# Performance work log

Hardware: AMD Instinct MI355X
Metric: run time of the kernel (lower is better)

The kernel has to match this reference:

```python
import jax, jax.numpy as jnp
import numpy as np

B, S, D_MODEL = 2, 2048, 1024
HID, D_FF, H, WIN = 256, 512, 4, 9
LN_EPS = 1e-5


def setup_inputs() -> dict:
    key = jax.random.key(0)
    ks = jax.random.split(key, 12)
    w = lambda k, shape: jax.random.normal(k, shape, jnp.float32) * 0.02
    return dict(
        q=jax.random.normal(ks[0], (B, S, D_MODEL), jnp.float32),
        k=jax.random.normal(ks[1], (B, S, D_MODEL), jnp.float32),
        v=jax.random.normal(ks[2], (B, S, D_MODEL), jnp.float32),
        Wq=w(ks[3], (D_MODEL, HID)), bq=jnp.zeros((HID,), jnp.float32),
        Wk=w(ks[4], (D_MODEL, HID)), bk=jnp.zeros((HID,), jnp.float32),
        Wv=w(ks[5], (D_MODEL, HID)), bv=jnp.zeros((HID,), jnp.float32),
        Wo=w(ks[6], (HID, D_MODEL)), bo=jnp.zeros((D_MODEL,), jnp.float32),
        alpha=jnp.zeros((1,), jnp.float32),
        adj_w=jnp.full((1,), 0.6, jnp.float32),
        adj_b=jnp.full((1,), 0.2, jnp.float32),
        W1=w(ks[7], (D_MODEL, D_FF)), b1=jnp.zeros((D_FF,), jnp.float32),
        W2=w(ks[8], (D_FF, D_MODEL)), b2=jnp.zeros((D_MODEL,), jnp.float32),
        g1=jnp.ones((D_MODEL,), jnp.float32), be1=jnp.zeros((D_MODEL,), jnp.float32),
        g2=jnp.ones((D_MODEL,), jnp.float32), be2=jnp.zeros((D_MODEL,), jnp.float32),
    )


def _layernorm(x, g, b):
    mu = jnp.mean(x, axis=-1, keepdims=True)
    var = jnp.mean((x - mu) ** 2, axis=-1, keepdims=True)
    return (x - mu) * jax.lax.rsqrt(var + LN_EPS) * g + b


def _signed_sqrt(x):
    # sqrt(relu(x)) - sqrt(relu(-x)) with torch-style zero grad on masked branch
    p = jnp.where(x > 0, jnp.sqrt(jnp.where(x > 0, x, 1.0)), 0.0)
    n = jnp.where(x < 0, jnp.sqrt(jnp.where(x < 0, -x, 1.0)), 0.0)
    return p - n


def _local_mask(seq_len, win):
    j = jnp.arange(seq_len)[:, None]              # [S,1]
    kk = jnp.arange(win)[None, :]                 # [1,W]
    idx = jnp.clip(j - win // 2 + kk, 0, seq_len - 1)
    m = jnp.zeros((seq_len, seq_len), jnp.float32)
    return m.at[jnp.broadcast_to(j, (seq_len, win)), idx].set(1.0)


def _forward(q, k, v, Wq, bq, Wk, bk, Wv, bv, Wo, bo, alpha, adj_w, adj_b,
             W1, b1, W2, b2, g1, be1, g2, be2):
    bs, seq, _ = q.shape
    dh = HID // H
    scale = 1.0 / np.sqrt(HID)

    Q = (q @ Wq + bq).reshape(bs, seq, H, dh).transpose(0, 2, 1, 3)  # [B,H,S,dh]
    K = (k @ Wk + bk).reshape(bs, seq, H, dh).transpose(0, 2, 1, 3)
    V = (v @ Wv + bv).reshape(bs, seq, H, dh).transpose(0, 2, 1, 3)

    # distance adjacency bias: exp(-|w*d^2 - b|), d = |i-j|
    i = jnp.arange(seq, dtype=jnp.float32)
    dist = jnp.abs(i[:, None] - i[None, :])
    adj = jnp.exp(-jnp.abs(adj_w[0] * dist ** 2 - adj_b[0]))  # [S,S]

    scores = jnp.einsum('bhqd,bhkd->bhqk', Q, K) * scale + adj  # [B,H,S,S]

    mask = _local_mask(seq, WIN)                                 # [S,S]
    l_scores = jnp.where(mask == 0, -1e9, scores)

    g_map = jax.nn.softmax(scores, axis=-1)
    l_map = jax.nn.softmax(l_scores, axis=-1)

    glb = jnp.einsum('bhqk,bhkd->bqhd', g_map, V).reshape(bs, seq, HID)
    lcl = jnp.einsum('bhqk,bhkd->bqhd', l_map, V).reshape(bs, seq, HID)

    a = jax.nn.sigmoid(alpha[0])
    tmp = a * glb + (1.0 - a) * lcl

    # norm_flag: signed sqrt then F.normalize (L2 along dim=1, eps=1e-12)
    tmp = _signed_sqrt(tmp)
    nrm = jnp.maximum(jnp.sqrt(jnp.sum(tmp ** 2, axis=1, keepdims=True)), 1e-12)
    tmp = tmp / nrm

    attn_out = tmp @ Wo + bo

    x = q + attn_out
    x = _layernorm(x, g1, be1)
    # FFN (dropout inactive in eval)
    x = x + (jax.nn.relu(x @ W1 + b1) @ W2 + b2)
    x = _layernorm(x, g2, be2)
    return x


def reference(q, k, v, Wq, bq, Wk, bk, Wv, bv, Wo, bo, alpha, adj_w, adj_b,
              W1, b1, W2, b2, g1, be1, g2, be2):
    return _forward(q, k, v, Wq, bq, Wk, bk, Wv, bv, Wo, bo, alpha, adj_w,
                    adj_b, W1, b1, W2, b2, g1, be1, g2, be2)
```

## Files before the change

kernel.cpp:

```cpp
#include <hip/hip_runtime.h>

#define B_SZ   2
#define S_LEN  2048
#define DMODEL 1024
#define HID    256
#define NH     4
#define DH     64
#define DFF    512
#define LN_EPS 1e-5f
#define ATT_SCALE 0.0625f

typedef __attribute__((ext_vector_type(8))) short bf16x8;
typedef __attribute__((ext_vector_type(4))) float f32x4;

static __device__ __forceinline__ unsigned short f2bf(float x) {
    union { float f; unsigned u; } v; v.f = x;
    unsigned r = v.u + 0x7FFFu + ((v.u >> 16) & 1u);
    return (unsigned short)(r >> 16);
}
static __device__ __forceinline__ unsigned packbf(float a, float b) {
    return (unsigned)f2bf(a) | ((unsigned)f2bf(b) << 16);
}
static __device__ __forceinline__ float bf2f(unsigned short h) {
    union { unsigned u; float f; } v; v.u = ((unsigned)h) << 16; return v.f;
}
static __device__ __forceinline__ int swz(int byte) {
    return byte ^ ((byte >> 3) & 0x70);
}

#if defined(__has_builtin)
#if __has_builtin(__builtin_amdgcn_global_load_lds)
#define HAVE_GLD 1
#endif
#endif

static __device__ __forceinline__ void gld16(const void* g, void* l) {
#ifdef HAVE_GLD
    __builtin_amdgcn_global_load_lds(
        (const __attribute__((address_space(1))) void*)g,
        (__attribute__((address_space(3))) void*)l, 16, 0, 0);
#else
    *(uint4*)((char*)l + (threadIdx.x & 63) * 16) = *(const uint4*)g;
#endif
}

__device__ __forceinline__ void stage_tile(const unsigned short* __restrict__ G,
                                           int row0, int k0, int K, char* lds, int t)
{
    #pragma unroll
    for (int i = 0; i < 2; ++i) {
        int ci = (t >> 6) * 2 + i;
        int o  = (ci * 64 + (t & 63)) * 16;
        int L  = o ^ ((o >> 3) & 0x70);
        const char* ga = (const char*)G +
            ((size_t)(row0 + (L >> 7)) * K + k0) * 2 + (L & 127);
        gld16(ga, lds + ci * 1024);
    }
}

__device__ __forceinline__ void compute_strip(const char* As, const char* Bs,
                                              f32x4 acc[4], int w, int lr, int lg)
{
    #pragma unroll
    for (int ks = 0; ks < 2; ++ks) {
        int koff = ks * 64 + lg * 16;
        bf16x8 bfv = *(const bf16x8*)(Bs + (((w * 16 + lr) * 128 + koff) ^ ((lr & 7) << 4)));
        #pragma unroll
        for (int m = 0; m < 4; ++m) {
            int r = m * 16 + lr;
            bf16x8 af = *(const bf16x8*)(As + ((r * 128 + koff) ^ ((lr & 7) << 4)));
            acc[m] = __builtin_amdgcn_mfma_f32_16x16x32_bf16(af, bfv, acc[m], 0, 0, 0);
        }
    }
}

__device__ __forceinline__ void gemm64_core(
    const unsigned short* __restrict__ A, const unsigned short* __restrict__ W,
    const float* __restrict__ bias, const float* __restrict__ residf,
    const unsigned short* __restrict__ residb,
    float* __restrict__ Cf, unsigned short* __restrict__ Cb,
    int N, int K, int relu, int row0, int col0)
{
    __shared__ char ldsb[32768];
    char* As0 = ldsb;          char* Bs0 = ldsb + 8192;
    char* As1 = ldsb + 16384;  char* Bs1 = ldsb + 24576;

    const int t = threadIdx.x;
    const int w = t >> 6, l = t & 63;
    const int lr = l & 15, lg = l >> 4;

    f32x4 acc[4] = {};

    stage_tile(A, row0, 0, K, As0, t);
    stage_tile(W, col0, 0, K, Bs0, t);
    __syncthreads();

    const int NK = K >> 6;
    int buf = 0;
    for (int ks = 0; ks < NK; ++ks) {
        if (ks + 1 < NK) {
            stage_tile(A, row0, (ks + 1) * 64, K, buf ? As0 : As1, t);
            stage_tile(W, col0, (ks + 1) * 64, K, buf ? Bs0 : Bs1, t);
        }
        compute_strip(buf ? As1 : As0, buf ? Bs1 : Bs0, acc, w, lr, lg);
        __syncthreads();
        buf ^= 1;
    }

    float* T = (float*)ldsb;
    #pragma unroll
    for (int m = 0; m < 4; ++m)
        #pragma unroll
        for (int r = 0; r < 4; ++r)
            T[(m * 16 + lg * 4 + r) * 65 + w * 16 + lr] =
                acc[m][r] + bias[col0 + w * 16 + lr];
    __syncthreads();

    #pragma unroll
    for (int i = 0; i < 4; ++i) {
        int idx = t + i * 256;
        int row = idx >> 4, c4 = idx & 15;
        float v0 = T[row * 65 + c4 * 4 + 0];
        float v1 = T[row * 65 + c4 * 4 + 1];
        float v2 = T[row * 65 + c4 * 4 + 2];
        float v3 = T[row * 65 + c4 * 4 + 3];
        size_t goff = (size_t)(row0 + row) * N + col0 + c4 * 4;
        if (residf) {
            float4 rv = *(const float4*)(residf + goff);
            v0 += rv.x; v1 += rv.y; v2 += rv.z; v3 += rv.w;
        }
        if (residb) {
            uint2 rb = *(const uint2*)(residb + goff);
            v0 += bf2f((unsigned short)(rb.x & 0xFFFF));
            v1 += bf2f((unsigned short)(rb.x >> 16));
            v2 += bf2f((unsigned short)(rb.y & 0xFFFF));
            v3 += bf2f((unsigned short)(rb.y >> 16));
        }
        if (relu) {
            v0 = fmaxf(v0, 0.f); v1 = fmaxf(v1, 0.f);
            v2 = fmaxf(v2, 0.f); v3 = fmaxf(v3, 0.f);
        }
        if (Cb) *(uint2*)(Cb + goff) = make_uint2(packbf(v0, v1), packbf(v2, v3));
        else    *(float4*)(Cf + goff) = make_float4(v0, v1, v2, v3);
    }
}

__global__ __launch_bounds__(256) void gemm_b16(
    const unsigned short* __restrict__ A, const unsigned short* __restrict__ W,
    const float* __restrict__ bias, const float* __restrict__ residf,
    const unsigned short* __restrict__ residb,
    float* __restrict__ Cf, unsigned short* __restrict__ Cb,
    int N, int K, int relu)
{
    gemm64_core(A, W, bias, residf, residb, Cf, Cb, N, K, relu,
                blockIdx.x * 64, blockIdx.y * 64);
}

__global__ __launch_bounds__(256) void gemm_qkv3(
    const unsigned short* __restrict__ qkvb, const unsigned short* __restrict__ Wt,
    const float* __restrict__ bq, const float* __restrict__ bk,
    const float* __restrict__ bv, unsigned short* __restrict__ outb)
{
    const int z = blockIdx.z;
    const unsigned short* A = qkvb + (size_t)z * 4096 * 1024;
    const unsigned short* W = Wt + (size_t)z * 262144;
    const float* bias = (z == 0) ? bq : ((z == 1) ? bk : bv);
    unsigned short* Cb = outb + (size_t)z * 4096 * 256;
    gemm64_core(A, W, bias, nullptr, nullptr, nullptr, Cb, 256, 1024, 0,
                blockIdx.x * 64, blockIdx.y * 64);
}

__global__ __launch_bounds__(256) void prep_w(
    const float* __restrict__ Wq, const float* __restrict__ Wk,
    const float* __restrict__ Wv, const float* __restrict__ Wo,
    const float* __restrict__ W1, const float* __restrict__ W2,
    unsigned short* __restrict__ Wt)
{
    __shared__ float tile[64][65];
    const int bid = blockIdx.x;
    const float* src; int K, N; size_t off; int local;
    if (bid < 64)       { src = Wq; K = 1024; N = 256;  off = 0;        local = bid; }
    else if (bid < 128) { src = Wk; K = 1024; N = 256;  off = 262144;  local = bid - 64; }
    else if (bid < 192) { src = Wv; K = 1024; N = 256;  off = 524288;  local = bid - 128; }
    else if (bid < 256) { src = Wo; K = 256;  N = 1024; off = 786432;  local = bid - 192; }
    else if (bid < 384) { src = W1; K = 1024; N = 512;  off = 1048576; local = bid - 256; }
    else                { src = W2; K = 512;  N = 1024; off = 1572864; local = bid - 384; }
    const int nkt = K >> 6;
    const int k0 = (local % nkt) * 64, n0 = (local / nkt) * 64;
    const int t = threadIdx.x;
    #pragma unroll
    for (int i = 0; i < 16; ++i) {
        int id = t + i * 256;
        int r = id >> 6, c = id & 63;
        tile[r][c] = src[(size_t)(k0 + r) * N + n0 + c];
    }
    __syncthreads();
    unsigned* Wt32 = (unsigned*)(Wt + off);
    #pragma unroll
    for (int i = 0; i < 8; ++i) {
        int id = t + i * 256;
        int n = id >> 5, ku = id & 31;
        Wt32[((size_t)(n0 + n) * K + k0) / 2 + ku] =
            packbf(tile[2 * ku][n], tile[2 * ku + 1][n]);
    }
}

__global__ __launch_bounds__(256) void prep_qkv(
    const float* __restrict__ q, const float* __restrict__ k,
    const float* __restrict__ v, unsigned short* __restrict__ qkvb)
{
    const float* src = blockIdx.z == 0 ? q : (blockIdx.z == 1 ? k : v);
    uint2* dst = (uint2*)(qkvb + (size_t)blockIdx.z * 4096 * 1024);
    int idx = blockIdx.x * 256 + threadIdx.x;
    float4 x = ((const float4*)src)[idx];
    dst[idx] = make_uint2(packbf(x.x, x.y), packbf(x.z, x.w));
}

__global__ __launch_bounds__(256) void prep_v(const unsigned short* __restrict__ Vb,
                                              unsigned short* __restrict__ Vt)
{
    __shared__ unsigned Vl[64][34];
    const int k0 = blockIdx.x * 64;
    const int bh = blockIdx.y;
    const int b = bh >> 2, h = bh & 3;
    const int t = threadIdx.x;
    const unsigned* Vg = (const unsigned*)Vb + (size_t)(b * S_LEN) * 128 + h * 32;
    #pragma unroll
    for (int i = 0; i < 8; ++i) {
        int id = t + i * 256;
        int key = id >> 5, cu = id & 31;
        Vl[key][cu] = Vg[(size_t)(k0 + key) * 128 + cu];
    }
    __syncthreads();
    const unsigned short* Vl16 = (const unsigned short*)Vl;
    unsigned* Vo = (unsigned*)Vt + (size_t)bh * 65536;
    #pragma unroll
    for (int i = 0; i < 8; ++i) {
        int id = t + i * 256;
        int d = id >> 5, ku = id & 31;
        unsigned lo = Vl16[(2 * ku) * 68 + d];
        unsigned hi = Vl16[(2 * ku + 1) * 68 + d];
        Vo[(size_t)d * 1024 + (k0 >> 1) + ku] = lo | (hi << 16);
    }
}

__global__ __launch_bounds__(256) void attn_global_split(
    const unsigned short* __restrict__ Qb, const unsigned short* __restrict__ Kb,
    const unsigned short* __restrict__ Vt, const float* __restrict__ adj_w,
    const float* __restrict__ adj_b, float* __restrict__ Opart,
    float* __restrict__ mlpart)
{
    __shared__ unsigned Kl[2048];
    __shared__ unsigned Vl[2048];
    __shared__ unsigned Pl[4][512];

    const int q0 = blockIdx.x * 64;
    const int bh = blockIdx.y;
    const int ck = blockIdx.z;
    const int b = bh >> 2, h = bh & 3;
    const int t = threadIdx.x;
    const int w = t >> 6, l = t & 63;
    const int lr = l & 15, lg = l >> 4;
    const float aw = adj_w[0], ab = adj_b[0];

    const int qrow = q0 + w * 16 + lr;
    const unsigned* qb32 = (const unsigned*)Qb + (size_t)(b * S_LEN + qrow) * 128 + h * 32;
    bf16x8 qf[2];
    #pragma unroll
    for (int hh = 0; hh < 2; ++hh) {
        union { unsigned u[4]; bf16x8 v; } tmpu;
        #pragma unroll
        for (int jj = 0; jj < 4; ++jj) tmpu.u[jj] = qb32[hh * 16 + lg * 4 + jj];
        qf[hh] = tmpu.v;
    }

    const unsigned* Kg = (const unsigned*)Kb + (size_t)(b * S_LEN) * 128 + h * 32;
    const unsigned* Vg = (const unsigned*)Vt + (size_t)bh * 65536;
    const int kbase = ck * 512;

    float mrow = -1e30f, lrow = 0.f;
    f32x4 o[4] = {};
    uint4 rk[2], rv[2];

    #pragma unroll
    for (int i = 0; i < 2; ++i) {
        int id4 = t + i * 256;
        int r4 = id4 >> 3, c4 = id4 & 7;
        rk[i] = *(const uint4*)(Kg + (size_t)(kbase + r4) * 128 + c4 * 4);
        rv[i] = *(const uint4*)(Vg + (size_t)r4 * 1024 + (kbase >> 1) + c4 * 4);
    }
    #pragma unroll
    for (int i = 0; i < 2; ++i) {
        int id4 = t + i * 256;
        int r4 = id4 >> 3, c4 = id4 & 7;
        *(uint4*)((char*)Kl + swz(r4 * 128 + c4 * 16)) = rk[i];
        *(uint4*)((char*)Vl + swz(r4 * 128 + c4 * 16)) = rv[i];
    }

    for (int tt = 0; tt < 8; ++tt) {
        const int k0 = kbase + tt * 64;
        __syncthreads();
        if (tt < 7) {
            const int kn = k0 + 64;
            #pragma unroll
            for (int i = 0; i < 2; ++i) {
                int id4 = t + i * 256;
                int r4 = id4 >> 3, c4 = id4 & 7;
                rk[i] = *(const uint4*)(Kg + (size_t)(kn + r4) * 128 + c4 * 4);
                rv[i] = *(const uint4*)(Vg + (size_t)r4 * 1024 + (kn >> 1) + c4 * 4);
            }
        }

        float sv[4][4];
        #pragma unroll
        for (int f = 0; f < 4; ++f) {
            int krow = f * 16 + lr;
            bf16x8 kf0 = *(const bf16x8*)((const char*)Kl + swz(krow * 128 + lg * 16));
            bf16x8 kf1 = *(const bf16x8*)((const char*)Kl + swz(krow * 128 + lg * 16 + 64));
            f32x4 stf = {0.f, 0.f, 0.f, 0.f};
            stf = __builtin_amdgcn_mfma_f32_16x16x32_bf16(kf0, qf[0], stf, 0, 0, 0);
            stf = __builtin_amdgcn_mfma_f32_16x16x32_bf16(kf1, qf[1], stf, 0, 0, 0);
            int klo = k0 + f * 16;
            bool near = (q0 + w * 16 + 15 >= klo - 6) && (q0 + w * 16 <= klo + 21);
            #pragma unroll
            for (int r = 0; r < 4; ++r) {
                float x = stf[r] * ATT_SCALE;
                if (near) {
                    int key = klo + lg * 4 + r;
                    float dd = (float)(qrow - key);
                    x += __expf(-fabsf(aw * dd * dd - ab));
                }
                sv[f][r] = x;
            }
        }

        float tmax = -1e30f;
        #pragma unroll
        for (int f = 0; f < 4; ++f)
            #pragma unroll
            for (int r = 0; r < 4; ++r) tmax = fmaxf(tmax, sv[f][r]);
        tmax = fmaxf(tmax, __shfl_xor(tmax, 16, 64));
        tmax = fmaxf(tmax, __shfl_xor(tmax, 32, 64));
        float mnew = fmaxf(mrow, tmax);
        float fac  = __expf(mrow - mnew);
        float ts = 0.f;
        #pragma unroll
        for (int f = 0; f < 4; ++f)
            #pragma unroll
            for (int r = 0; r < 4; ++r) {
                float p = __expf(sv[f][r] - mnew);
                sv[f][r] = p; ts += p;
            }
        ts += __shfl_xor(ts, 16, 64);
        ts += __shfl_xor(ts, 32, 64);
        lrow = lrow * fac + ts;
        mrow = mnew;
        #pragma unroll
        for (int rf = 0; rf < 4; ++rf) o[rf] *= fac;

        #pragma unroll
        for (int f = 0; f < 4; ++f) {
            uint2 pw;
            pw.x = packbf(sv[f][0], sv[f][1]);
            pw.y = packbf(sv[f][2], sv[f][3]);
            *(uint2*)((char*)Pl[w] + swz(lr * 128 + f * 32 + lg * 8)) = pw;
        }

        #pragma unroll
        for (int hh = 0; hh < 2; ++hh) {
            bf16x8 pf = *(const bf16x8*)((const char*)Pl[w] + swz(lr * 128 + lg * 16 + 64 * hh));
            #pragma unroll
            for (int rf = 0; rf < 4; ++rf) {
                int vrow = rf * 16 + lr;
                bf16x8 vf = *(const bf16x8*)((const char*)Vl + swz(vrow * 128 + lg * 16 + 64 * hh));
                o[rf] = __builtin_amdgcn_mfma_f32_16x16x32_bf16(vf, pf, o[rf], 0, 0, 0);
            }
        }

        __syncthreads();
        if (tt < 7) {
            #pragma unroll
            for (int i = 0; i < 2; ++i) {
                int id4 = t + i * 256;
                int r4 = id4 >> 3, c4 = id4 & 7;
                *(uint4*)((char*)Kl + swz(r4 * 128 + c4 * 16)) = rk[i];
                *(uint4*)((char*)Vl + swz(r4 * 128 + c4 * 16)) = rv[i];
            }
        }
    }

    const size_t idx = (size_t)(ck * 8 + bh) * 2048 + qrow;
    float* op = Opart + idx * 64;
    #pragma unroll
    for (int rf = 0; rf < 4; ++rf)
        *(float4*)(op + rf * 16 + lg * 4) = make_float4(o[rf][0], o[rf][1], o[rf][2], o[rf][3]);
    if (lg == 0) {
        mlpart[idx * 2]     = mrow;
        mlpart[idx * 2 + 1] = lrow;
    }
}

__global__ __launch_bounds__(256) void attn_combine(
    const float* __restrict__ Opart, const float* __restrict__ mlpart,
    const unsigned short* __restrict__ lcl_b, const float* __restrict__ alpha,
    unsigned short* __restrict__ tmpb)
{
    const int row = blockIdx.x;
    const int b = row >> 11;
    const int w = threadIdx.x >> 6;
    const int lane = threadIdx.x & 63;
    const size_t base = (size_t)(b * NH + w) * 2048 + (row & 2047);

    float mv[4], lv[4];
    float M = -1e30f;
    #pragma unroll
    for (int ck = 0; ck < 4; ++ck) {
        mv[ck] = mlpart[(ck * 16384 + base) * 2];
        lv[ck] = mlpart[(ck * 16384 + base) * 2 + 1];
        M = fmaxf(M, mv[ck]);
    }
    float O = 0.f, L = 0.f;
    #pragma unroll
    for (int ck = 0; ck < 4; ++ck) {
        float e = __expf(mv[ck] - M);
        O += e * Opart[(ck * 16384 + base) * 64 + lane];
        L += e * lv[ck];
    }
    float g = O / L;
    float lval = bf2f(lcl_b[(size_t)row * HID + w * 64 + lane]);
    float a = 1.f / (1.f + expf(-alpha[0]));
    float x = a * g + (1.f - a) * lval;
    float r = x > 0.f ? sqrtf(x) : (x < 0.f ? -sqrtf(-x) : 0.f);
    tmpb[(size_t)row * HID + w * 64 + lane] = f2bf(r);
}

__global__ __launch_bounds__(256) void attn_local(
    const unsigned short* __restrict__ Qb, const unsigned short* __restrict__ Kb,
    const unsigned short* __restrict__ Vb, const float* __restrict__ adj_w,
    const float* __restrict__ adj_b, unsigned short* __restrict__ lcl_b)
{
    const int wave = threadIdx.x >> 6;
    const int lane = threadIdx.x & 63;
    const int gr = blockIdx.x * 4 + wave;
    const int b = gr >> 13;
    const int rem = gr & 8191;
    const int h = rem >> 11;
    const int i = rem & 2047;
    const float w = adj_w[0], bb = adj_b[0];

    const float qd = bf2f(Qb[(size_t)(b * S_LEN + i) * HID + h * 64 + lane]);

    float sc[9]; int cls[9];
    float mx = -1e30f; int prev = -1;
    #pragma unroll
    for (int kk = 0; kk < 9; ++kk) {
        int c = i - 4 + kk;
        c = c < 0 ? 0 : (c > S_LEN - 1 ? S_LEN - 1 : c);
        bool valid = (c != prev);
        prev = c;
        float kd = bf2f(Kb[(size_t)(b * S_LEN + c) * HID + h * 64 + lane]);
        float part = qd * kd;
        #pragma unroll
        for (int off = 32; off; off >>= 1) part += __shfl_xor(part, off, 64);
        float dd = fabsf((float)(i - c));
        float vv = part * ATT_SCALE + expf(-fabsf(w * dd * dd - bb));
        sc[kk]  = valid ? vv : -1e30f;
        cls[kk] = c;
        mx = fmaxf(mx, sc[kk]);
    }
    float sum = 0.f;
    #pragma unroll
    for (int kk = 0; kk < 9; ++kk) { sc[kk] = expf(sc[kk] - mx); sum += sc[kk]; }
    const float inv = 1.f / sum;
    float o = 0.f;
    #pragma unroll
    for (int kk = 0; kk < 9; ++kk)
        o += sc[kk] * bf2f(Vb[(size_t)(b * S_LEN + cls[kk]) * HID + h * 64 + lane]);

    lcl_b[((size_t)(b * S_LEN + i)) * HID + h * 64 + lane] = f2bf(o * inv);
}

__global__ __launch_bounds__(256) void colnorm_part(
    const unsigned short* __restrict__ tmpb, float* __restrict__ part)
{
    __shared__ unsigned short Tl[16][256];
    const int b = blockIdx.x >> 7, ch = blockIdx.x & 127;
    const int t = threadIdx.x;
    const uint4* src = (const uint4*)(tmpb + ((size_t)b * S_LEN + ch * 16) * HID);
    #pragma unroll
    for (int i = 0; i < 2; ++i) {
        int idx = t + i * 256;
        ((uint4*)Tl)[idx] = src[idx];
    }
    __syncthreads();
    float ss = 0.f;
    #pragma unroll
    for (int r = 0; r < 16; ++r) {
        float v2 = bf2f(Tl[r][t]);
        ss += v2 * v2;
    }
    part[blockIdx.x * 256 + t] = ss;
}

__global__ __launch_bounds__(64) void colnorm_fin(
    const float* __restrict__ part, float* __restrict__ inv_nrm)
{
    const int bc = blockIdx.x;
    const int b = bc >> 8, c = bc & 255;
    const int j = threadIdx.x;
    float s = part[(b * 128 + j) * 256 + c] + part[(b * 128 + j + 64) * 256 + c];
    #pragma unroll
    for (int off = 32; off; off >>= 1) s += __shfl_xor(s, off, 64);
    if (j == 0) inv_nrm[bc] = 1.f / fmaxf(sqrtf(s), 1e-12f);
}

__global__ __launch_bounds__(256) void scale_inv(
    unsigned short* __restrict__ tmpb, const float* __restrict__ inv_nrm)
{
    int idx = blockIdx.x * 256 + threadIdx.x;
    int c = idx & 255, b = idx >> 19;
    tmpb[idx] = f2bf(bf2f(tmpb[idx]) * inv_nrm[b * 256 + c]);
}

__global__ __launch_bounds__(256) void layernorm_k(
    const float* __restrict__ x, const float* __restrict__ g,
    const float* __restrict__ be, float* __restrict__ outf,
    unsigned short* __restrict__ outb)
{
    const int row = blockIdx.x;
    const float4 xv = ((const float4*)(x + (size_t)row * DMODEL))[threadIdx.x];
    float s  = xv.x + xv.y + xv.z + xv.w;
    float ss = xv.x * xv.x + xv.y * xv.y + xv.z * xv.z + xv.w * xv.w;
    #pragma unroll
    for (int off = 32; off; off >>= 1) {
        s  += __shfl_xor(s,  off, 64);
        ss += __shfl_xor(ss, off, 64);
    }
    __shared__ float rs[4], rss[4];
    if ((threadIdx.x & 63) == 0) { rs[threadIdx.x >> 6] = s; rss[threadIdx.x >> 6] = ss; }
    __syncthreads();
    s  = rs[0] + rs[1] + rs[2] + rs[3];
    ss = rss[0] + rss[1] + rss[2] + rss[3];
    const float mu  = s * (1.f / DMODEL);
    const float var = ss * (1.f / DMODEL) - mu * mu;
    const float r   = rsqrtf(var + LN_EPS);
    const float4 gv = ((const float4*)g)[threadIdx.x];
    const float4 bv = ((const float4*)be)[threadIdx.x];
    float4 ov;
    ov.x = (xv.x - mu) * r * gv.x + bv.x;
    ov.y = (xv.y - mu) * r * gv.y + bv.y;
    ov.z = (xv.z - mu) * r * gv.z + bv.z;
    ov.w = (xv.w - mu) * r * gv.w + bv.w;
    if (outf) ((float4*)(outf + (size_t)row * DMODEL))[threadIdx.x] = ov;
    if (outb) {
        unsigned* ob = (unsigned*)(outb + (size_t)row * DMODEL);
        ob[threadIdx.x * 2]     = packbf(ov.x, ov.y);
        ob[threadIdx.x * 2 + 1] = packbf(ov.z, ov.w);
    }
}

extern "C" void kernel_launch(void* const* d_in, const int* in_sizes, int n_in,
                              void* d_out, int out_size, void* d_ws, size_t ws_size,
                              hipStream_t stream)
{
    const float* q     = (const float*)d_in[0];
    const float* k     = (const float*)d_in[1];
    const float* v     = (const float*)d_in[2];
    const float* Wq    = (const float*)d_in[3];
    const float* bq    = (const float*)d_in[4];
    const float* Wk    = (const float*)d_in[5];
    const float* bk    = (const float*)d_in[6];
    const float* Wv    = (const float*)d_in[7];
    const float* bv    = (const float*)d_in[8];
    const float* Wo    = (const float*)d_in[9];
    const float* bo    = (const float*)d_in[10];
    const float* alpha = (const float*)d_in[11];
    const float* adj_w = (const float*)d_in[12];
    const float* adj_b = (const float*)d_in[13];
    const float* W1    = (const float*)d_in[14];
    const float* b1    = (const float*)d_in[15];
    const float* W2    = (const float*)d_in[16];
    const float* b2    = (const float*)d_in[17];
    const float* g1    = (const float*)d_in[18];
    const float* be1   = (const float*)d_in[19];
    const float* g2    = (const float*)d_in[20];
    const float* be2   = (const float*)d_in[21];

    const int ROWS = B_SZ * S_LEN;

    char* WS = (char*)d_ws;
    float*          x1     = (float*)WS;
    float*          Opart  = (float*)WS;
    unsigned short* qkvb   = (unsigned short*)WS;
    float*          mlpart = (float*)(WS + (16u << 20));
    unsigned short* xlnb   = (unsigned short*)(WS + (16u << 20));
    unsigned short* lcl_b  = (unsigned short*)(WS + (26u << 20));
    unsigned short* Qb     = (unsigned short*)(WS + (28u << 20));
    unsigned short* Kb     = (unsigned short*)(WS + (30u << 20));
    unsigned short* Vb     = (unsigned short*)(WS + (32u << 20));
    unsigned short* Vt     = (unsigned short*)(WS + (34u << 20));
    unsigned short* tmpb   = (unsigned short*)(WS + (36u << 20));
    float*          invn   = (float*)(WS + (38u << 20));
    float*          part   = (float*)(WS + (38u << 20) + 4096);
    unsigned short* Wt     = (unsigned short*)(WS + (39u << 20));
    unsigned short* hbufb  = (unsigned short*)(WS + (28u << 20));

    prep_w<<<dim3(512), dim3(256), 0, stream>>>(Wq, Wk, Wv, Wo, W1, W2, Wt);
    prep_qkv<<<dim3(4096, 1, 3), dim3(256), 0, stream>>>(q, k, v, qkvb);
    gemm_qkv3<<<dim3(64, 4, 3), dim3(256), 0, stream>>>(qkvb, Wt, bq, bk, bv, Qb);
    prep_v<<<dim3(32, 8), dim3(256), 0, stream>>>(Vb, Vt);
    attn_global_split<<<dim3(32, 8, 4), dim3(256), 0, stream>>>(Qb, Kb, Vt, adj_w, adj_b,
                                                                Opart, mlpart);
    attn_local<<<dim3(4096), dim3(256), 0, stream>>>(Qb, Kb, Vb, adj_w, adj_b, lcl_b);
    attn_combine<<<dim3(4096), dim3(256), 0, stream>>>(Opart, mlpart, lcl_b, alpha, tmpb);
    colnorm_part<<<dim3(256), dim3(256), 0, stream>>>(tmpb, part);
    colnorm_fin<<<dim3(512), dim3(64), 0, stream>>>(part, invn);
    scale_inv<<<dim3(4096), dim3(256), 0, stream>>>(tmpb, invn);
    gemm_b16<<<dim3(64, 16), dim3(256), 0, stream>>>(tmpb, Wt + 786432, bo, q, nullptr,
                                                     x1, nullptr, DMODEL, HID, 0);
    layernorm_k<<<dim3(ROWS), dim3(256), 0, stream>>>(x1, g1, be1, nullptr, xlnb);
    gemm_b16<<<dim3(64, 8), dim3(256), 0, stream>>>(xlnb, Wt + 1048576, b1, nullptr, nullptr,
                                                    nullptr, hbufb, DFF, DMODEL, 1);
    gemm_b16<<<dim3(64, 16), dim3(256), 0, stream>>>(hbufb, Wt + 1572864, b2, nullptr, xlnb,
                                                     x1, nullptr, DMODEL, DFF, 0);
    layernorm_k<<<dim3(ROWS), dim3(256), 0, stream>>>(x1, g2, be2, (float*)d_out, nullptr);
}
```

Measured before the change: 268.3 us.

## Fuse local attention into combine, remap global-attention blocks, stage output via LDS

Merges the local windowed-attention kernel into the split-combine kernel, so the intermediate local result buffer is never written or re-read and one launch goes away. The global-attention grid is flattened to 1D with a swizzled block-to-tile mapping (bid&7 major) that groups blocks differently across XCDs/L2 for K/V reuse. Partial outputs are staged through shared memory and written as fully coalesced rows instead of scattered float4 stores. This costs extra syncthreads and a larger combine kernel with more registers.

```diff
diff --git a/kernel.cpp b/kernel.cpp
--- a/kernel.cpp
+++ b/kernel.cpp
@@ -250,13 +250,16 @@
     const float* __restrict__ adj_b, float* __restrict__ Opart,
     float* __restrict__ mlpart)
 {
-    __shared__ unsigned Kl[2048];
-    __shared__ unsigned Vl[2048];
-    __shared__ unsigned Pl[4][512];
-
-    const int q0 = blockIdx.x * 64;
-    const int bh = blockIdx.y;
-    const int ck = blockIdx.z;
+    __shared__ unsigned shmem[6144];
+    unsigned* Kl = shmem;
+    unsigned* Vl = shmem + 2048;
+    unsigned* Pl = shmem + 4096;
+
+    const int bid = blockIdx.x;
+    const int lid = (bid & 7) * 128 + (bid >> 3);
+    const int q0 = (lid & 31) * 64;
+    const int bh = (lid >> 5) & 7;
+    const int ck = lid >> 8;
     const int b = bh >> 2, h = bh & 3;
     const int t = threadIdx.x;
     const int w = t >> 6, l = t & 63;
@@ -363,12 +366,12 @@
             uint2 pw;
             pw.x = packbf(sv[f][0], sv[f][1]);
             pw.y = packbf(sv[f][2], sv[f][3]);
-            *(uint2*)((char*)Pl[w] + swz(lr * 128 + f * 32 + lg * 8)) = pw;
+            *(uint2*)((char*)(Pl + w * 512) + swz(lr * 128 + f * 32 + lg * 8)) = pw;
         }
 
         #pragma unroll
         for (int hh = 0; hh < 2; ++hh) {
-            bf16x8 pf = *(const bf16x8*)((const char*)Pl[w] + swz(lr * 128 + lg * 16 + 64 * hh));
+            bf16x8 pf = *(const bf16x8*)((const char*)(Pl + w * 512) + swz(lr * 128 + lg * 16 + 64 * hh));
             #pragma unroll
             for (int rf = 0; rf < 4; ++rf) {
                 int vrow = rf * 16 + lr;
@@ -376,7 +379,6 @@
                 o[rf] = __builtin_amdgcn_mfma_f32_16x16x32_bf16(vf, pf, o[rf], 0, 0, 0);
             }
         }
-
         __syncthreads();
         if (tt < 7) {
             #pragma unroll
@@ -390,71 +392,48 @@
     }
 
     const size_t idx = (size_t)(ck * 8 + bh) * 2048 + qrow;
-    float* op = Opart + idx * 64;
-    #pragma unroll
-    for (int rf = 0; rf < 4; ++rf)
-        *(float4*)(op + rf * 16 + lg * 4) = make_float4(o[rf][0], o[rf][1], o[rf][2], o[rf][3]);
     if (lg == 0) {
         mlpart[idx * 2]     = mrow;
         mlpart[idx * 2 + 1] = lrow;
     }
+
+    __syncthreads();
+    float* T = (float*)shmem;
+    #pragma unroll
+    for (int rf = 0; rf < 4; ++rf)
+        *(float4*)(T + (w * 16 + lr) * 68 + rf * 16 + lg * 4) =
+            make_float4(o[rf][0], o[rf][1], o[rf][2], o[rf][3]);
+    __syncthreads();
+    float* obase = Opart + ((size_t)(ck * 8 + bh) * 2048 + q0) * 64;
+    #pragma unroll
+    for (int i = 0; i < 4; ++i) {
+        int id = t + i * 256;
+        int row = id >> 4, c4 = id & 15;
+        *(float4*)(obase + row * 64 + c4 * 4) =
+            *(const float4*)(T + row * 68 + c4 * 4);
+    }
 }
 
 __global__ __launch_bounds__(256) void attn_combine(
     const float* __restrict__ Opart, const float* __restrict__ mlpart,
-    const unsigned short* __restrict__ lcl_b, const float* __restrict__ alpha,
+    const unsigned short* __restrict__ Qb, const unsigned short* __restrict__ Kb,
+    const unsigned short* __restrict__ Vb, const float* __restrict__ alpha,
+    const float* __restrict__ adj_w, const float* __restrict__ adj_b,
     unsigned short* __restrict__ tmpb)
 {
     const int row = blockIdx.x;
     const int b = row >> 11;
-    const int w = threadIdx.x >> 6;
+    const int s = row & 2047;
+    const int h = threadIdx.x >> 6;
     const int lane = threadIdx.x & 63;
-    const size_t base = (size_t)(b * NH + w) * 2048 + (row & 2047);
-
-    float mv[4], lv[4];
-    float M = -1e30f;
-    #pragma unroll
-    for (int ck = 0; ck < 4; ++ck) {
-        mv[ck] = mlpart[(ck * 16384 + base) * 2];
-        lv[ck] = mlpart[(ck * 16384 + base) * 2 + 1];
-        M = fmaxf(M, mv[ck]);
-    }
-    float O = 0.f, L = 0.f;
-    #pragma unroll
-    for (int ck = 0; ck < 4; ++ck) {
-        float e = __expf(mv[ck] - M);
-        O += e * Opart[(ck * 16384 + base) * 64 + lane];
-        L += e * lv[ck];
-    }
-    float g = O / L;
-    float lval = bf2f(lcl_b[(size_t)row * HID + w * 64 + lane]);
-    float a = 1.f / (1.f + expf(-alpha[0]));
-    float x = a * g + (1.f - a) * lval;
-    float r = x > 0.f ? sqrtf(x) : (x < 0.f ? -sqrtf(-x) : 0.f);
-    tmpb[(size_t)row * HID + w * 64 + lane] = f2bf(r);
-}
-
-__global__ __launch_bounds__(256) void attn_local(
-    const unsigned short* __restrict__ Qb, const unsigned short* __restrict__ Kb,
-    const unsigned short* __restrict__ Vb, const float* __restrict__ adj_w,
-    const float* __restrict__ adj_b, unsigned short* __restrict__ lcl_b)
-{
-    const int wave = threadIdx.x >> 6;
-    const int lane = threadIdx.x & 63;
-    const int gr = blockIdx.x * 4 + wave;
-    const int b = gr >> 13;
-    const int rem = gr & 8191;
-    const int h = rem >> 11;
-    const int i = rem & 2047;
     const float w = adj_w[0], bb = adj_b[0];
 
-    const float qd = bf2f(Qb[(size_t)(b * S_LEN + i) * HID + h * 64 + lane]);
-
+    const float qd = bf2f(Qb[(size_t)row * HID + h * 64 + lane]);
     float sc[9]; int cls[9];
     float mx = -1e30f; int prev = -1;
     #pragma unroll
     for (int kk = 0; kk < 9; ++kk) {
-        int c = i - 4 + kk;
+        int c = s - 4 + kk;
         c = c < 0 ? 0 : (c > S_LEN - 1 ? S_LEN - 1 : c);
         bool valid = (c != prev);
         prev = c;
@@ -462,7 +441,7 @@
         float part = qd * kd;
         #pragma unroll
         for (int off = 32; off; off >>= 1) part += __shfl_xor(part, off, 64);
-        float dd = fabsf((float)(i - c));
+        float dd = fabsf((float)(s - c));
         float vv = part * ATT_SCALE + expf(-fabsf(w * dd * dd - bb));
         sc[kk]  = valid ? vv : -1e30f;
         cls[kk] = c;
@@ -471,13 +450,33 @@
     float sum = 0.f;
     #pragma unroll
     for (int kk = 0; kk < 9; ++kk) { sc[kk] = expf(sc[kk] - mx); sum += sc[kk]; }
-    const float inv = 1.f / sum;
-    float o = 0.f;
+    float lval = 0.f;
     #pragma unroll
     for (int kk = 0; kk < 9; ++kk)
-        o += sc[kk] * bf2f(Vb[(size_t)(b * S_LEN + cls[kk]) * HID + h * 64 + lane]);
-
-    lcl_b[((size_t)(b * S_LEN + i)) * HID + h * 64 + lane] = f2bf(o * inv);
+        lval += sc[kk] * bf2f(Vb[(size_t)(b * S_LEN + cls[kk]) * HID + h * 64 + lane]);
+    lval /= sum;
+
+    const size_t base = (size_t)(b * NH + h) * 2048 + s;
+    float mv[4], lv[4];
+    float M = -1e30f;
+    #pragma unroll
+    for (int ck = 0; ck < 4; ++ck) {
+        mv[ck] = mlpart[(ck * 16384 + base) * 2];
+        lv[ck] = mlpart[(ck * 16384 + base) * 2 + 1];
+        M = fmaxf(M, mv[ck]);
+    }
+    float O = 0.f, L = 0.f;
+    #pragma unroll
+    for (int ck = 0; ck < 4; ++ck) {
+        float e = __expf(mv[ck] - M);
+        O += e * Opart[(ck * 16384 + base) * 64 + lane];
+        L += e * lv[ck];
+    }
+    float g = O / L;
+    float a = 1.f / (1.f + expf(-alpha[0]));
+    float x = a * g + (1.f - a) * lval;
+    float r = x > 0.f ? sqrtf(x) : (x < 0.f ? -sqrtf(-x) : 0.f);
+    tmpb[(size_t)row * HID + h * 64 + lane] = f2bf(r);
 }
 
 __global__ __launch_bounds__(256) void colnorm_part(
@@ -594,7 +593,6 @@
     unsigned short* qkvb   = (unsigned short*)WS;
     float*          mlpart = (float*)(WS + (16u << 20));
     unsigned short* xlnb   = (unsigned short*)(WS + (16u << 20));
-    unsigned short* lcl_b  = (unsigned short*)(WS + (26u << 20));
     unsigned short* Qb     = (unsigned short*)(WS + (28u << 20));
     unsigned short* Kb     = (unsigned short*)(WS + (30u << 20));
     unsigned short* Vb     = (unsigned short*)(WS + (32u << 20));
@@ -609,10 +607,10 @@
     prep_qkv<<<dim3(4096, 1, 3), dim3(256), 0, stream>>>(q, k, v, qkvb);
     gemm_qkv3<<<dim3(64, 4, 3), dim3(256), 0, stream>>>(qkvb, Wt, bq, bk, bv, Qb);
     prep_v<<<dim3(32, 8), dim3(256), 0, stream>>>(Vb, Vt);
-    attn_global_split<<<dim3(32, 8, 4), dim3(256), 0, stream>>>(Qb, Kb, Vt, adj_w, adj_b,
-                                                                Opart, mlpart);
-    attn_local<<<dim3(4096), dim3(256), 0, stream>>>(Qb, Kb, Vb, adj_w, adj_b, lcl_b);
-    attn_combine<<<dim3(4096), dim3(256), 0, stream>>>(Opart, mlpart, lcl_b, alpha, tmpb);
+    attn_global_split<<<dim3(1024), dim3(256), 0, stream>>>(Qb, Kb, Vt, adj_w, adj_b,
+                                                            Opart, mlpart);
+    attn_combine<<<dim3(4096), dim3(256), 0, stream>>>(Opart, mlpart, Qb, Kb, Vb,
+                                                       alpha, adj_w, adj_b, tmpb);
     colnorm_part<<<dim3(256), dim3(256), 0, stream>>>(tmpb, part);
     colnorm_fin<<<dim3(512), dim3(64), 0, stream>>>(part, invn);
     scale_inv<<<dim3(4096), dim3(256), 0, stream>>>(tmpb, invn);
```

Measured after the change: 261.7 us. 1.03x faster.
